# Performance work log

Measured on AMD Instinct MI355X. Metric: run time of the kernel, lower is better.

## Reference

```python
import jax, jax.numpy as jnp
import numpy as np

N, K, D = 256, 16, 1024
EPS = 1e-06


def setup_inputs() -> dict:
    key = jax.random.key(0)
    k1, k2, k3, k4 = jax.random.split(key, 4)
    scale = 0.05  # keep pairwise distances in a non-saturated logit range
    return {
        'image_features': jax.random.normal(k1, (N, K, D), jnp.float32) * scale,
        'caption_features': jax.random.normal(k2, (N, K, D), jnp.float32) * scale,
        'image_logsigma': jax.random.normal(k3, (N, D), jnp.float32),
        'caption_logsigma': jax.random.normal(k4, (N, D), jnp.float32),
        'negative_scale': jnp.full((1,), 5.0, jnp.float32),
        'shift': jnp.full((1,), 5.0, jnp.float32),
    }


def _pairwise_cdist(x, y):
    # dist[i, j, k, l] = || x[i, k] - y[j, l] ||_2, computed via Gram expansion
    # to avoid materializing the (N, N, K, K, D) broadcast-difference tensor.
    x2 = jnp.sum(x * x, axis=-1)  # (N, K)
    y2 = jnp.sum(y * y, axis=-1)  # (N, K)
    xy = jnp.einsum('ikd,jld->ijkl', x, y)  # (N, N, K, K)
    sq = x2[:, None, :, None] + y2[None, :, None, :] - 2.0 * xy
    sq = jnp.maximum(sq, 0.0)
    return jnp.sqrt(sq + EPS)


def _nll_sum(dist, negative_scale, shift):
    # dist: (N, N, K, K) -> logits (N, N, K*K)
    n = dist.shape[0]
    kk = dist.shape[2] * dist.shape[3]
    logits = (-negative_scale[0] * dist + shift[0]).reshape(n, n, kk)
    matched = jnp.where(jnp.eye(n, dtype=bool), 1.0, -1.0)[:, :, None]  # (N, N, 1)
    # logsumexp over the stacked (logit, -logit) pair == logaddexp(l, -l)
    inner = logits * matched - jnp.logaddexp(logits, -logits)
    nll = -jax.scipy.special.logsumexp(inner, axis=-1) + jnp.log(jnp.float32(kk))  # (N, N)
    return jnp.sum(nll)  # pos (diag) + neg (off-diag) sums


def reference(image_features, caption_features, image_logsigma, caption_logsigma,
              negative_scale, shift):
    # uniform_lambda = 0, vib_beta = 0 -> loss = i2t + t2i soft-contrastive NLL
    dist = _pairwise_cdist(image_features, caption_features)  # (N, N, K, K)
    i2t = _nll_sum(dist, negative_scale, shift)
    # t2i: anchors/candidates swapped -> transposed pair grid (same per-pair set)
    t2i = _nll_sum(jnp.transpose(dist, (1, 0, 3, 2)), negative_scale, shift)
    return i2t + t2i
```

## Files before the change

### kernel.cpp

```cpp
#include <hip/hip_runtime.h>
#include <hip/hip_bf16.h>
#include <cstdint>


using f32x4 = __attribute__((ext_vector_type(4))) float;
using s16x8 = __attribute__((ext_vector_type(8))) short;

#define DDIM   1024
#define BM     256
#define BN     256
#define BK     32
#define NT     32
#define LOGKK  5.5451774444795625f
#define DEPS   1e-6f

__device__ __forceinline__ void gload16(const void* g, void* l) {
  __builtin_amdgcn_global_load_lds((const __attribute__((address_space(1))) void*)g,
                                   (__attribute__((address_space(3))) void*)l, 16, 0, 0);
}

__device__ __forceinline__ unsigned short bf16_rne(float x) {
  uint32_t u = __builtin_bit_cast(uint32_t, x);
  uint32_t r = (u + 0x7FFFu + ((u >> 16) & 1u)) >> 16;
  return (unsigned short)r;
}

__global__ __launch_bounds__(256) void mcsc_prep(
    const float* __restrict__ img, const float* __restrict__ cap,
    unsigned short* __restrict__ Xhi, unsigned short* __restrict__ Yhi,
    float* __restrict__ x2, float* __restrict__ y2, float* __restrict__ out)
{
  int w = blockIdx.x * 4 + (threadIdx.x >> 6);
  int lane = threadIdx.x & 63;
  int isY = w >> 12;
  int row = w & 4095;
  const float* src = (isY ? cap : img) + (size_t)row * DDIM;
  unsigned short* dst = (isY ? Yhi : Xhi) + (size_t)row * DDIM;

  float s = 0.f;
#pragma unroll
  for (int j = 0; j < 4; ++j) {
    int col = (j * 64 + lane) * 4;
    float4 v = *(const float4*)(src + col);
    const float* vp = (const float*)&v;
    unsigned short h[4];
#pragma unroll
    for (int e = 0; e < 4; ++e) { float x = vp[e]; s += x * x; h[e] = bf16_rne(x); }
    *(ushort4*)(dst + col) = make_ushort4(h[0], h[1], h[2], h[3]);
  }
#pragma unroll
  for (int off = 32; off >= 1; off >>= 1) s += __shfl_xor(s, off);
  if (lane == 0) (isY ? y2 : x2)[row] = s;
  if (w == 0 && lane == 0) out[0] = 0.f;
}

__global__ __launch_bounds__(512, 2) void mcsc_main(
    const unsigned short* __restrict__ Xhi, const unsigned short* __restrict__ Yhi,
    const float* __restrict__ x2, const float* __restrict__ y2,
    const float* __restrict__ nsp, const float* __restrict__ shp,
    float* __restrict__ out)
{
  __shared__ __align__(16) char lds[4 * 32768];
  __shared__ float redBuf[8];

  int bid = blockIdx.x;
  int wg = (bid & 7) * 32 + (bid >> 3);
  int bm = wg >> 4, bn = wg & 15;
  int rowBase = bm * BM, colBase = bn * BN;

  int t = threadIdx.x;
  int wid = t >> 6, lane = t & 63;
  int lr = lane & 15, lk = lane >> 4;
  int wr = wid >> 2, wc = wid & 3;
  int waveRow = wr * 128, waveCol = wc * 64;

  f32x4 acc[8][4] = {};

  int srow = wid * 16 + (lane >> 2);
  int scol = ((lane & 3) ^ ((lane >> 3) & 3)) * 16;
  const char* aSrc = (const char*)(Xhi + (size_t)(rowBase + srow) * DDIM) + scol;
  const char* bSrc = (const char*)(Yhi + (size_t)(colBase + srow) * DDIM) + scol;
  int ldsDst = wid * 1024;

  auto stage = [&](int ks, int s) {
    int ko = ks * 64;
    char* base = lds + s * 32768;
#pragma unroll
    for (int i = 0; i < 2; ++i) {
      gload16(aSrc + (size_t)(i * 128) * 2048 + ko, base + i * 8192 + ldsDst);
      gload16(bSrc + (size_t)(i * 128) * 2048 + ko, base + 16384 + i * 8192 + ldsDst);
    }
  };

  int rdoff = (lk * 16) ^ (((lr >> 1) & 3) << 4);
  int aOff = (waveRow + lr) * 64 + rdoff;
  int bOff = 16384 + (waveCol + lr) * 64 + rdoff;

  stage(0, 0); stage(1, 1); stage(2, 2);

  for (int ks = 0; ks < NT; ++ks) {
    int cur = ks & 3;
    if (ks < NT - 2)       asm volatile("s_waitcnt vmcnt(8)" ::: "memory");
    else if (ks == NT - 2) asm volatile("s_waitcnt vmcnt(4)" ::: "memory");
    else                   asm volatile("s_waitcnt vmcnt(0)" ::: "memory");
    __builtin_amdgcn_s_barrier();
    __builtin_amdgcn_sched_barrier(0);

    if (ks + 3 < NT) stage(ks + 3, (ks + 3) & 3);

    const char* sBase = lds + cur * 32768;
    s16x8 af[8], bf[4];
#pragma unroll
    for (int m = 0; m < 8; ++m)
      af[m] = *(const s16x8*)(sBase + aOff + m * 1024);
#pragma unroll
    for (int n = 0; n < 4; ++n)
      bf[n] = *(const s16x8*)(sBase + bOff + n * 1024);
#pragma unroll
    for (int m = 0; m < 8; ++m)
#pragma unroll
      for (int n = 0; n < 4; ++n)
        acc[m][n] = __builtin_amdgcn_mfma_f32_16x16x32_bf16(af[m], bf[n], acc[m][n], 0, 0, 0);
  }

  float ns = nsp[0], sh = shp[0];
  float waveAcc = 0.f;
#pragma unroll
  for (int m = 0; m < 8; ++m) {
    int gr0 = rowBase + waveRow + m * 16;
    f32x4 x2v = *(const f32x4*)(x2 + gr0 + lk * 4);
#pragma unroll
    for (int n = 0; n < 4; ++n) {
      int gc0 = colBase + waveCol + n * 16;
      bool diag = ((gr0 >> 4) == (gc0 >> 4));
      float y2c = y2[gc0 + lr];
      float ts = 0.f;
#pragma unroll
      for (int r = 0; r < 4; ++r) {
        float sq = x2v[r] + y2c - 2.f * acc[m][n][r];
        sq = fmaxf(sq, 0.f);
        float dd = __fsqrt_rn(sq + DEPS);
        float l = sh - ns * dd;
        float a = diag ? (2.f * l) : (-2.f * l);
        ts += 1.f / (1.f + __expf(-a));
      }
#pragma unroll
      for (int off = 32; off >= 1; off >>= 1) ts += __shfl_xor(ts, off);
      waveAcc += (LOGKK - __logf(ts));
    }
  }
  if (lane == 0) redBuf[wid] = waveAcc;
  __syncthreads();
  if (t == 0) {
    float bs = redBuf[0] + redBuf[1] + redBuf[2] + redBuf[3]
             + redBuf[4] + redBuf[5] + redBuf[6] + redBuf[7];
    atomicAdd(out, 2.f * bs);
  }
}

extern "C" void kernel_launch(void* const* d_in, const int* in_sizes, int n_in,
                              void* d_out, int out_size, void* d_ws, size_t ws_size,
                              hipStream_t stream) {
  const float* img = (const float*)d_in[0];
  const float* cap = (const float*)d_in[1];
  const float* nsp = (const float*)d_in[4];
  const float* shp = (const float*)d_in[5];
  float* out = (float*)d_out;

  char* ws = (char*)d_ws;
  unsigned short* Xhi = (unsigned short*)(ws + (size_t)0);
  unsigned short* Yhi = (unsigned short*)(ws + (size_t)8 * 1024 * 1024);
  float* x2 = (float*)(ws + (size_t)16 * 1024 * 1024);
  float* y2 = (float*)(ws + (size_t)16 * 1024 * 1024 + 16384);

  mcsc_prep<<<dim3(2048), dim3(256), 0, stream>>>(img, cap, Xhi, Yhi, x2, y2, out);
  mcsc_main<<<dim3(256), dim3(512), 0, stream>>>(Xhi, Yhi, x2, y2, nsp, shp, out);
}
```

Measured before the change: 139.5 us.

## Shrink GEMM tile to 256x128 with 512 blocks and 3-stage pipeline

Halves the column tile so the main kernel launches 512 workgroups of 4 waves instead of 256 workgroups of 8 waves. This is meant to fill all CUs of the MI355X, which has more than 256. The LDS ring drops from four 32KB stages to three 24KB slots, with prefetch depth two, so two blocks fit per CU. Blocks are also remapped into XCD-local regions to improve L2 reuse of the X and Y panels. The cost is lower reuse of the A tile per loaded byte and a shallower prefetch, which may expose more memory latency.

```diff
diff --git a/kernel.cpp b/kernel.cpp
--- a/kernel.cpp
+++ b/kernel.cpp
@@ -8,9 +8,10 @@
 
 #define DDIM   1024
 #define BM     256
-#define BN     256
+#define BN     128
 #define BK     32
 #define NT     32
+#define SLOT   24576
 #define LOGKK  5.5451774444795625f
 #define DEPS   1e-6f
 
@@ -54,61 +55,64 @@
   if (w == 0 && lane == 0) out[0] = 0.f;
 }
 
-__global__ __launch_bounds__(512, 2) void mcsc_main(
+__global__ __launch_bounds__(256, 2) void mcsc_main(
     const unsigned short* __restrict__ Xhi, const unsigned short* __restrict__ Yhi,
     const float* __restrict__ x2, const float* __restrict__ y2,
     const float* __restrict__ nsp, const float* __restrict__ shp,
     float* __restrict__ out)
 {
-  __shared__ __align__(16) char lds[4 * 32768];
-  __shared__ float redBuf[8];
+  __shared__ __align__(16) char lds[3 * SLOT];
+  __shared__ float redBuf[4];
 
   int bid = blockIdx.x;
-  int wg = (bid & 7) * 32 + (bid >> 3);
-  int bm = wg >> 4, bn = wg & 15;
+  int xcd = bid & 7, k = bid >> 3;
+  int region = xcd + 8 * (k >> 5);
+  int idx = k & 31;
+  int bm = (region >> 2) * 4 + (idx >> 3);
+  int bn = (region & 3) * 8 + (idx & 7);
   int rowBase = bm * BM, colBase = bn * BN;
 
   int t = threadIdx.x;
   int wid = t >> 6, lane = t & 63;
   int lr = lane & 15, lk = lane >> 4;
-  int wr = wid >> 2, wc = wid & 3;
+  int wr = wid >> 1, wc = wid & 1;
   int waveRow = wr * 128, waveCol = wc * 64;
 
   f32x4 acc[8][4] = {};
 
-  int srow = wid * 16 + (lane >> 2);
-  int scol = ((lane & 3) ^ ((lane >> 3) & 3)) * 16;
+  int srow = t >> 2;
+  int scol = ((t & 3) ^ ((t >> 3) & 3)) * 16;
   const char* aSrc = (const char*)(Xhi + (size_t)(rowBase + srow) * DDIM) + scol;
   const char* bSrc = (const char*)(Yhi + (size_t)(colBase + srow) * DDIM) + scol;
   int ldsDst = wid * 1024;
 
   auto stage = [&](int ks, int s) {
     int ko = ks * 64;
-    char* base = lds + s * 32768;
+    char* base = lds + s * SLOT;
 #pragma unroll
-    for (int i = 0; i < 2; ++i) {
-      gload16(aSrc + (size_t)(i * 128) * 2048 + ko, base + i * 8192 + ldsDst);
-      gload16(bSrc + (size_t)(i * 128) * 2048 + ko, base + 16384 + i * 8192 + ldsDst);
-    }
+    for (int i = 0; i < 4; ++i)
+      gload16(aSrc + (size_t)(i * 64) * 2048 + ko, base + i * 4096 + ldsDst);
+#pragma unroll
+    for (int i = 0; i < 2; ++i)
+      gload16(bSrc + (size_t)(i * 64) * 2048 + ko, base + 16384 + i * 4096 + ldsDst);
   };
 
   int rdoff = (lk * 16) ^ (((lr >> 1) & 3) << 4);
   int aOff = (waveRow + lr) * 64 + rdoff;
   int bOff = 16384 + (waveCol + lr) * 64 + rdoff;
 
-  stage(0, 0); stage(1, 1); stage(2, 2);
+  stage(0, 0); stage(1, 1);
 
   for (int ks = 0; ks < NT; ++ks) {
-    int cur = ks & 3;
-    if (ks < NT - 2)       asm volatile("s_waitcnt vmcnt(8)" ::: "memory");
-    else if (ks == NT - 2) asm volatile("s_waitcnt vmcnt(4)" ::: "memory");
-    else                   asm volatile("s_waitcnt vmcnt(0)" ::: "memory");
+    int cur = ks % 3;
+    if (ks < NT - 1) asm volatile("s_waitcnt vmcnt(6)" ::: "memory");
+    else             asm volatile("s_waitcnt vmcnt(0)" ::: "memory");
     __builtin_amdgcn_s_barrier();
     __builtin_amdgcn_sched_barrier(0);
 
-    if (ks + 3 < NT) stage(ks + 3, (ks + 3) & 3);
+    if (ks + 2 < NT) stage(ks + 2, (ks + 2) % 3);
 
-    const char* sBase = lds + cur * 32768;
+    const char* sBase = lds + cur * SLOT;
     s16x8 af[8], bf[4];
 #pragma unroll
     for (int m = 0; m < 8; ++m)
@@ -152,8 +156,7 @@
   if (lane == 0) redBuf[wid] = waveAcc;
   __syncthreads();
   if (t == 0) {
-    float bs = redBuf[0] + redBuf[1] + redBuf[2] + redBuf[3]
-             + redBuf[4] + redBuf[5] + redBuf[6] + redBuf[7];
+    float bs = redBuf[0] + redBuf[1] + redBuf[2] + redBuf[3];
     atomicAdd(out, 2.f * bs);
   }
 }
@@ -174,5 +177,5 @@
   float* y2 = (float*)(ws + (size_t)16 * 1024 * 1024 + 16384);
 
   mcsc_prep<<<dim3(2048), dim3(256), 0, stream>>>(img, cap, Xhi, Yhi, x2, y2, out);
-  mcsc_main<<<dim3(256), dim3(512), 0, stream>>>(Xhi, Yhi, x2, y2, nsp, shp, out);
+  mcsc_main<<<dim3(512), dim3(256), 0, stream>>>(Xhi, Yhi, x2, y2, nsp, shp, out);
 }
```

Measured after the change: 135.1 us. 3.1% less time.

## Split K-step into two half phases with interleaved prefetch and setprio

Applied to the files above, without the earlier changes.

Each K iteration now runs in two phases. Each phase loads half the A fragments, issues half of the next stage's global-to-LDS prefetch, then runs 16 MFMAs under raised wave priority, with barriers between phases. The aim is to overlap LDS reads and global loads with MFMA work across the two waves per SIMD, in a ping-pong style schedule, and to reduce register pressure from holding all fragments at once. The change adds more barriers per iteration, and the vmcnt bookkeeping has to match the split issue order exactly.

```diff
diff --git a/kernel.cpp b/kernel.cpp
--- a/kernel.cpp
+++ b/kernel.cpp
@@ -82,45 +82,68 @@
   const char* bSrc = (const char*)(Yhi + (size_t)(colBase + srow) * DDIM) + scol;
   int ldsDst = wid * 1024;
 
-  auto stage = [&](int ks, int s) {
+  auto stage_half = [&](int ks, int s, int h) {
     int ko = ks * 64;
     char* base = lds + s * 32768;
-#pragma unroll
-    for (int i = 0; i < 2; ++i) {
-      gload16(aSrc + (size_t)(i * 128) * 2048 + ko, base + i * 8192 + ldsDst);
-      gload16(bSrc + (size_t)(i * 128) * 2048 + ko, base + 16384 + i * 8192 + ldsDst);
-    }
+    gload16(aSrc + (size_t)(h * 128) * 2048 + ko, base + h * 8192 + ldsDst);
+    gload16(bSrc + (size_t)(h * 128) * 2048 + ko, base + 16384 + h * 8192 + ldsDst);
   };
 
   int rdoff = (lk * 16) ^ (((lr >> 1) & 3) << 4);
   int aOff = (waveRow + lr) * 64 + rdoff;
   int bOff = 16384 + (waveCol + lr) * 64 + rdoff;
 
-  stage(0, 0); stage(1, 1); stage(2, 2);
+  stage_half(0, 0, 0); stage_half(0, 0, 1);
+  stage_half(1, 1, 0); stage_half(1, 1, 1);
+  stage_half(2, 2, 0); stage_half(2, 2, 1);
+  asm volatile("s_waitcnt vmcnt(8)" ::: "memory");
+  __builtin_amdgcn_s_barrier();
 
   for (int ks = 0; ks < NT; ++ks) {
     int cur = ks & 3;
-    if (ks < NT - 2)       asm volatile("s_waitcnt vmcnt(8)" ::: "memory");
-    else if (ks == NT - 2) asm volatile("s_waitcnt vmcnt(4)" ::: "memory");
-    else                   asm volatile("s_waitcnt vmcnt(0)" ::: "memory");
-    __builtin_amdgcn_s_barrier();
-    __builtin_amdgcn_sched_barrier(0);
-
-    if (ks + 3 < NT) stage(ks + 3, (ks + 3) & 3);
-
     const char* sBase = lds + cur * 32768;
-    s16x8 af[8], bf[4];
-#pragma unroll
-    for (int m = 0; m < 8; ++m)
+    bool more = (ks + 3 < NT);
+    int nslot = (ks + 3) & 3;
+
+    s16x8 af[4], bf[4];
+#pragma unroll
+    for (int m = 0; m < 4; ++m)
       af[m] = *(const s16x8*)(sBase + aOff + m * 1024);
 #pragma unroll
     for (int n = 0; n < 4; ++n)
       bf[n] = *(const s16x8*)(sBase + bOff + n * 1024);
-#pragma unroll
-    for (int m = 0; m < 8; ++m)
+    if (more) stage_half(ks + 3, nslot, 0);
+    __builtin_amdgcn_s_barrier();
+    asm volatile("s_waitcnt lgkmcnt(0)" ::: "memory");
+    __builtin_amdgcn_sched_barrier(0);
+    __builtin_amdgcn_s_setprio(1);
+#pragma unroll
+    for (int m = 0; m < 4; ++m)
 #pragma unroll
       for (int n = 0; n < 4; ++n)
         acc[m][n] = __builtin_amdgcn_mfma_f32_16x16x32_bf16(af[m], bf[n], acc[m][n], 0, 0, 0);
+    __builtin_amdgcn_s_setprio(0);
+    __builtin_amdgcn_s_barrier();
+
+    s16x8 ag[4];
+#pragma unroll
+    for (int m = 0; m < 4; ++m)
+      ag[m] = *(const s16x8*)(sBase + aOff + (m + 4) * 1024);
+    if (more) stage_half(ks + 3, nslot, 1);
+    if (ks < 29)       asm volatile("s_waitcnt vmcnt(8)" ::: "memory");
+    else if (ks == 29) asm volatile("s_waitcnt vmcnt(4)" ::: "memory");
+    else if (ks == 30) asm volatile("s_waitcnt vmcnt(0)" ::: "memory");
+    __builtin_amdgcn_s_barrier();
+    asm volatile("s_waitcnt lgkmcnt(0)" ::: "memory");
+    __builtin_amdgcn_sched_barrier(0);
+    __builtin_amdgcn_s_setprio(1);
+#pragma unroll
+    for (int m = 0; m < 4; ++m)
+#pragma unroll
+      for (int n = 0; n < 4; ++n)
+        acc[m + 4][n] = __builtin_amdgcn_mfma_f32_16x16x32_bf16(ag[m], bf[n], acc[m + 4][n], 0, 0, 0);
+    __builtin_amdgcn_s_setprio(0);
+    __builtin_amdgcn_s_barrier();
   }
 
   float ns = nsp[0], sh = shp[0];
```

Measured after the change: 132.3 us. 5.2% less time.
